# Performance work log

Measured on AMD Instinct MI355X. Metric: run time of the kernel, lower is better.

## Reference

```python
import jax, jax.numpy as jnp
import numpy as np

B, L, A, D = 16, 1024, 512, 1024


def setup_inputs() -> dict:
    key = jax.random.key(0)
    ks = jax.random.split(key, 12)
    s = 1.0 / np.sqrt(D)
    s2 = 1.0 / np.sqrt(2 * D)
    return {
        "text_features": jax.random.normal(ks[0], (B, L, D), jnp.float32),
        "audio_features": jax.random.normal(ks[1], (B, A, D), jnp.float32),
        "Wt1": jax.random.uniform(ks[2], (D, D), jnp.float32, -s, s),
        "bt1": jax.random.uniform(ks[3], (D,), jnp.float32, -s, s),
        "Wa1": jax.random.uniform(ks[4], (D, D), jnp.float32, -s, s),
        "w_att1": jax.random.uniform(ks[5], (2 * D,), jnp.float32, -s2, s2),
        "b_att1": jax.random.uniform(ks[6], (), jnp.float32, -s2, s2),
        "Wt2": jax.random.uniform(ks[7], (D, D), jnp.float32, -s, s),
        "Wa2": jax.random.uniform(ks[8], (D, D), jnp.float32, -s, s),
        "ba2": jax.random.uniform(ks[9], (D,), jnp.float32, -s, s),
        "w_att2": jax.random.uniform(ks[10], (2 * D,), jnp.float32, -s2, s2),
        "b_att2": jax.random.uniform(ks[11], (), jnp.float32, -s2, s2),
    }


def reference(text_features, audio_features, Wt1, bt1, Wa1, w_att1, b_att1,
              Wt2, Wa2, ba2, w_att2, b_att2):
    # Additive co-attention. tanh(cat([u_i, v_j])) = cat([tanh(u_i), tanh(v_j)]),
    # so the post-tanh linear score decomposes into an outer sum — exact same math
    # as the naive repeat/cat/tanh/linear, without the (B,L,A,2D) intermediate.
    d = Wt1.shape[0]
    # --- attention over audio regions ---
    u1 = jnp.tanh(jnp.einsum('bld,ed->ble', text_features, Wt1) + bt1)   # (B,L,D)
    v1 = jnp.tanh(jnp.einsum('bad,ed->bae', audio_features, Wa1))        # (B,A,D)
    scores1 = (u1 @ w_att1[:d])[:, :, None] + (v1 @ w_att1[d:])[:, None, :] + b_att1  # (B,L,A)
    audio_att = jax.nn.softmax(scores1, axis=-1)
    att_audio_features = jnp.einsum('bla,bad->bld', audio_att, audio_features)  # (B,L,D)
    # --- attention over text positions (self.args.max_seq_len == L) ---
    u2 = jnp.tanh(jnp.einsum('bld,ed->ble', att_audio_features, Wa2) + ba2)  # (B,L,D)
    v2 = jnp.tanh(jnp.einsum('bkd,ed->bke', text_features, Wt2))             # (B,L,D)
    scores2 = (u2 @ w_att2[:d])[:, :, None] + (v2 @ w_att2[d:])[:, None, :] + b_att2  # (B,L,L)
    textual_att = jax.nn.softmax(scores2, axis=-1)
    att_text_features = jnp.einsum('blk,bkd->bld', textual_att, text_features)
    return (att_text_features, att_audio_features)
```

## Files before the change

### kernel.cpp

```cpp
#include <hip/hip_runtime.h>

typedef unsigned short u16;
typedef float f32x4 __attribute__((ext_vector_type(4)));
typedef int   i32x4 __attribute__((ext_vector_type(4)));
typedef u16   u16x8 __attribute__((ext_vector_type(8)));

#define SWZ(i) ((i) ^ ((((i) >> 6) & 3) << 3))

__device__ __forceinline__ u16 f2bf(float f) {
  unsigned u = __float_as_uint(f);
  u += 0x7FFFu + ((u >> 16) & 1u);
  return (u16)(u >> 16);
}

__device__ __forceinline__ int cvt_pk_bf16(float lo, float hi) {
  int r;
  asm("v_cvt_pk_bf16_f32 %0, %1, %2" : "=v"(r) : "v"(lo), "v"(hi));
  return r;
}

__device__ __forceinline__ float tanh_fast(float x) {
  float e = __expf(2.0f * x);
  return 1.0f - 2.0f / (e + 1.0f);
}

__device__ __forceinline__ void mfma_bf16(f32x4& acc, i32x4 a, i32x4 b) {
  asm("v_mfma_f32_16x16x32_bf16 %0, %1, %2, %0" : "+v"(acc) : "v"(a), "v"(b));
}

__global__ __launch_bounds__(256) void wcast_kernel(
    const float* __restrict__ w2, const float* __restrict__ w1,
    u16* __restrict__ w2b, u16* __restrict__ w1b) {
  int i = blockIdx.x * 256 + threadIdx.x;
  const float* src; u16* dst; int j;
  if (i < 131072) { src = w2; dst = w2b; j = i; }
  else            { src = w1; dst = w1b; j = i - 131072; }
  const float4* s = (const float4*)src;
  float4 a = s[2 * j], b = s[2 * j + 1];
  u16x8 o;
  o[0] = f2bf(a.x); o[1] = f2bf(a.y); o[2] = f2bf(a.z); o[3] = f2bf(a.w);
  o[4] = f2bf(b.x); o[5] = f2bf(b.y); o[6] = f2bf(b.z); o[7] = f2bf(b.w);
  *(u16x8*)(dst + (size_t)8 * j) = o;
}

__global__ __launch_bounds__(256) void score_kernel(
    const float* __restrict__ audio, const u16* __restrict__ w1b,
    const float* __restrict__ wva, float* __restrict__ sva,
    const float* __restrict__ text, const u16* __restrict__ w2b,
    const float* __restrict__ wvt, float* __restrict__ svt) {
  __shared__ u16 At[128 * 32];
  __shared__ u16 Bt[128 * 32];

  int bx = blockIdx.x;
  const float* Xf; const u16* Wb_; const float* wv; float* svout; int mt, split, M;
  if (bx < 256) {
    Xf = audio; Wb_ = w1b; wv = wva; svout = sva; M = 8192;
    mt = (bx & 7) * 8 + (bx >> 5); split = (bx >> 3) & 3;
  } else {
    int x = bx - 256;
    Xf = text; Wb_ = w2b; wv = wvt; svout = svt; M = 16384;
    mt = (x & 7) * 16 + (x >> 5); split = (x >> 3) & 3;
  }

  const int t = threadIdx.x;
  const int wid = t >> 6, lane = t & 63;
  const int wm = wid >> 1, wn = wid & 1;
  const int lane15 = lane & 15, lg = lane >> 4;
  const size_t m_base = (size_t)mt * 128;

  float rs[4][4];
  #pragma unroll
  for (int mi = 0; mi < 4; ++mi)
    #pragma unroll
    for (int r = 0; r < 4; ++r) rs[mi][r] = 0.f;

  const int ar0 = t >> 2,        ac0 = (t & 3) * 8;
  const int ar1 = (256 + t) >> 2, ac1 = (t & 3) * 8;
  const int wiA0 = SWZ(ar0 * 32 + ac0), wiA1 = SWZ(ar1 * 32 + ac1);

  const float* Xb = Xf + m_base * 1024;

  for (int nt = 0; nt < 2; ++nt) {
    const int n0 = split * 256 + nt * 128;

    f32x4 acc[4][4];
    #pragma unroll
    for (int mi = 0; mi < 4; ++mi)
      #pragma unroll
      for (int ni = 0; ni < 4; ++ni)
        acc[mi][ni] = (f32x4){0.f, 0.f, 0.f, 0.f};

    const u16* Wp = Wb_ + (size_t)n0 * 1024;

    float4 xa0 = *(const float4*)(Xb + (size_t)ar0 * 1024 + ac0);
    float4 xa0b = *(const float4*)(Xb + (size_t)ar0 * 1024 + ac0 + 4);
    float4 xa1 = *(const float4*)(Xb + (size_t)ar1 * 1024 + ac1);
    float4 xa1b = *(const float4*)(Xb + (size_t)ar1 * 1024 + ac1 + 4);
    i32x4 rb0 = *(const i32x4*)(Wp + (size_t)ar0 * 1024 + ac0);
    i32x4 rb1 = *(const i32x4*)(Wp + (size_t)ar1 * 1024 + ac1);

    for (int kt = 0; kt < 32; ++kt) {
      i32x4 wa0, wa1;
      wa0[0] = cvt_pk_bf16(xa0.x, xa0.y);  wa0[1] = cvt_pk_bf16(xa0.z, xa0.w);
      wa0[2] = cvt_pk_bf16(xa0b.x, xa0b.y); wa0[3] = cvt_pk_bf16(xa0b.z, xa0b.w);
      wa1[0] = cvt_pk_bf16(xa1.x, xa1.y);  wa1[1] = cvt_pk_bf16(xa1.z, xa1.w);
      wa1[2] = cvt_pk_bf16(xa1b.x, xa1b.y); wa1[3] = cvt_pk_bf16(xa1b.z, xa1b.w);
      __syncthreads();
      *(i32x4*)(At + wiA0) = wa0;
      *(i32x4*)(At + wiA1) = wa1;
      *(i32x4*)(Bt + wiA0) = rb0;
      *(i32x4*)(Bt + wiA1) = rb1;
      __syncthreads();
      if (kt < 31) {
        const int k1 = (kt + 1) * 32;
        xa0  = *(const float4*)(Xb + (size_t)ar0 * 1024 + k1 + ac0);
        xa0b = *(const float4*)(Xb + (size_t)ar0 * 1024 + k1 + ac0 + 4);
        xa1  = *(const float4*)(Xb + (size_t)ar1 * 1024 + k1 + ac1);
        xa1b = *(const float4*)(Xb + (size_t)ar1 * 1024 + k1 + ac1 + 4);
        rb0  = *(const i32x4*)(Wp + (size_t)ar0 * 1024 + k1 + ac0);
        rb1  = *(const i32x4*)(Wp + (size_t)ar1 * 1024 + k1 + ac1);
      }
      i32x4 af[4], bfr[4];
      #pragma unroll
      for (int mi = 0; mi < 4; ++mi) {
        int rr = wm * 64 + mi * 16 + lane15;
        af[mi] = *(const i32x4*)(At + SWZ(rr * 32 + lg * 8));
      }
      #pragma unroll
      for (int ni = 0; ni < 4; ++ni) {
        int rr = wn * 64 + ni * 16 + lane15;
        bfr[ni] = *(const i32x4*)(Bt + SWZ(rr * 32 + lg * 8));
      }
      #pragma unroll
      for (int mi = 0; mi < 4; ++mi)
        #pragma unroll
        for (int ni = 0; ni < 4; ++ni)
          mfma_bf16(acc[mi][ni], af[mi], bfr[ni]);
    }

    float wvn[4];
    #pragma unroll
    for (int ni = 0; ni < 4; ++ni) wvn[ni] = wv[n0 + wn * 64 + ni * 16 + lane15];
    #pragma unroll
    for (int mi = 0; mi < 4; ++mi)
      #pragma unroll
      for (int ni = 0; ni < 4; ++ni)
        #pragma unroll
        for (int r = 0; r < 4; ++r)
          rs[mi][r] += tanh_fast(acc[mi][ni][r]) * wvn[ni];
  }

  __syncthreads();
  float* sred = (float*)At;
  #pragma unroll
  for (int mi = 0; mi < 4; ++mi)
    #pragma unroll
    for (int r = 0; r < 4; ++r) {
      float v = rs[mi][r];
      v += __shfl_xor(v, 1);
      v += __shfl_xor(v, 2);
      v += __shfl_xor(v, 4);
      v += __shfl_xor(v, 8);
      if (lane15 == 0) sred[wn * 128 + wm * 64 + mi * 16 + lg * 4 + r] = v;
    }
  __syncthreads();
  if (t < 128) svout[(size_t)split * M + m_base + t] = sred[t] + sred[128 + t];
}

__global__ __launch_bounds__(256) void softq_bcast_kernel(
    const float* __restrict__ xA, const float* __restrict__ svA,
    const float* __restrict__ xT, const float* __restrict__ svT,
    float* __restrict__ out) {
  int bx = blockIdx.x;
  int stage = bx >> 8;
  int b = (bx >> 4) & 15, dch = bx & 15;
  int Acnt = stage ? 1024 : 512;
  int M = stage ? 16384 : 8192;
  const float* x = stage ? xT : xA;
  const float* svp = stage ? svT : svA;
  int rowbase = b * Acnt;

  __shared__ float p[1024];
  __shared__ float red[256];
  __shared__ float chunk[64];
  int t = threadIdx.x;

  float mloc = -1e30f;
  for (int a = t; a < Acnt; a += 256) {
    float v = svp[rowbase + a] + svp[M + rowbase + a] +
              svp[2 * M + rowbase + a] + svp[3 * M + rowbase + a];
    p[a] = v;
    mloc = fmaxf(mloc, v);
  }
  #pragma unroll
  for (int off = 32; off; off >>= 1) mloc = fmaxf(mloc, __shfl_xor(mloc, off));
  if ((t & 63) == 0) red[t >> 6] = mloc;
  __syncthreads();
  float mx = fmaxf(fmaxf(red[0], red[1]), fmaxf(red[2], red[3]));

  float sloc = 0.f;
  for (int a = t; a < Acnt; a += 256) {
    float e = __expf(p[a] - mx);
    p[a] = e;
    sloc += e;
  }
  #pragma unroll
  for (int off = 32; off; off >>= 1) sloc += __shfl_xor(sloc, off);
  __syncthreads();
  if ((t & 63) == 0) red[t >> 6] = sloc;
  __syncthreads();
  float inv = 1.0f / (red[0] + red[1] + red[2] + red[3]);

  int dl = t & 63, ag = t >> 6;
  const float* xb = x + (size_t)rowbase * 1024 + dch * 64 + dl;
  float acc = 0.f;
  #pragma unroll 8
  for (int a = ag; a < Acnt; a += 4) acc += p[a] * xb[(size_t)a * 1024];
  __syncthreads();
  red[t] = acc;
  __syncthreads();
  if (t < 64) {
    float tot = red[t] + red[t + 64] + red[t + 128] + red[t + 192];
    chunk[t] = tot * inv;
  }
  __syncthreads();

  size_t base4 = ((stage ? (size_t)0 : (size_t)16777216) +
                  (size_t)b * 1048576 + (size_t)dch * 64) >> 2;
  f32x4* o4 = (f32x4*)out;
  f32x4 v = ((f32x4*)chunk)[t & 15];
  int q = t & 15;
  #pragma unroll 4
  for (int l = t >> 4; l < 1024; l += 16)
    __builtin_nontemporal_store(v, &o4[base4 + (size_t)l * 256 + q]);
}

extern "C" void kernel_launch(void* const* d_in, const int* in_sizes, int n_in,
                              void* d_out, int out_size, void* d_ws, size_t ws_size,
                              hipStream_t stream) {
  const float* text  = (const float*)d_in[0];
  const float* audio = (const float*)d_in[1];
  const float* Wa1   = (const float*)d_in[4];
  const float* watt1 = (const float*)d_in[5];
  const float* Wt2   = (const float*)d_in[7];
  const float* watt2 = (const float*)d_in[10];

  char* ws = (char*)d_ws;
  u16*   w2b = (u16*)(ws);
  u16*   w1b = (u16*)(ws + 2097152);
  float* sv2 = (float*)(ws + 4194304);
  float* sv1 = (float*)(ws + 4456448);

  wcast_kernel<<<1024, 256, 0, stream>>>(Wt2, Wa1, w2b, w1b);

  score_kernel<<<768, 256, 0, stream>>>(audio, w1b, watt1 + 1024, sv1,
                                        text, w2b, watt2 + 1024, sv2);

  softq_bcast_kernel<<<512, 256, 0, stream>>>(audio, sv1, text, sv2, (float*)d_out);
}
```

Before: 352.9 us.

## Double-buffer score GEMM LDS tiles and split N across twice as many blocks

The score kernel now stages its A and B tiles in double-buffered shared memory, so each k-step needs one barrier instead of two and the next tile's conversion and store overlap the current MFMAs. Each block now covers a single 128-wide N tile instead of two, which doubles the grid to 1536 blocks and produces 8 partial score vectors per row instead of 4. The softmax kernel sums the 8 partials and the workspace offset for the audio scores moves to fit them. The change also asks for 4 blocks per CU through launch bounds and drops the old block-index swizzle. In exchange, shared memory per block doubles, the X tile is re-read by twice as many blocks, and the partial-sum traffic doubles.

```diff
diff --git a/kernel.cpp b/kernel.cpp
--- a/kernel.cpp
+++ b/kernel.cpp
@@ -43,114 +43,120 @@
   *(u16x8*)(dst + (size_t)8 * j) = o;
 }
 
-__global__ __launch_bounds__(256) void score_kernel(
+__global__ __launch_bounds__(256, 4) void score_kernel(
     const float* __restrict__ audio, const u16* __restrict__ w1b,
     const float* __restrict__ wva, float* __restrict__ sva,
     const float* __restrict__ text, const u16* __restrict__ w2b,
     const float* __restrict__ wvt, float* __restrict__ svt) {
-  __shared__ u16 At[128 * 32];
-  __shared__ u16 Bt[128 * 32];
+  __shared__ u16 At[2][4096];
+  __shared__ u16 Bt[2][4096];
 
   int bx = blockIdx.x;
   const float* Xf; const u16* Wb_; const float* wv; float* svout; int mt, split, M;
-  if (bx < 256) {
+  if (bx < 512) {
     Xf = audio; Wb_ = w1b; wv = wva; svout = sva; M = 8192;
-    mt = (bx & 7) * 8 + (bx >> 5); split = (bx >> 3) & 3;
+    split = bx >> 6; mt = bx & 63;
   } else {
-    int x = bx - 256;
+    int x = bx - 512;
     Xf = text; Wb_ = w2b; wv = wvt; svout = svt; M = 16384;
-    mt = (x & 7) * 16 + (x >> 5); split = (x >> 3) & 3;
-  }
+    split = x >> 7; mt = x & 127;
+  }
+  const int n0 = split * 128;
 
   const int t = threadIdx.x;
   const int wid = t >> 6, lane = t & 63;
   const int wm = wid >> 1, wn = wid & 1;
   const int lane15 = lane & 15, lg = lane >> 4;
-  const size_t m_base = (size_t)mt * 128;
-
-  float rs[4][4];
+
+  const int ar0 = t >> 2,         ac0 = (t & 3) * 8;
+  const int ar1 = (256 + t) >> 2, ac1 = (t & 3) * 8;
+  const int wi0 = SWZ(ar0 * 32 + ac0), wi1 = SWZ(ar1 * 32 + ac1);
+
+  const float* Xb = Xf + (size_t)mt * 128 * 1024;
+  const u16*   Wp = Wb_ + (size_t)n0 * 1024;
+
+  f32x4 acc[4][4];
   #pragma unroll
   for (int mi = 0; mi < 4; ++mi)
     #pragma unroll
-    for (int r = 0; r < 4; ++r) rs[mi][r] = 0.f;
-
-  const int ar0 = t >> 2,        ac0 = (t & 3) * 8;
-  const int ar1 = (256 + t) >> 2, ac1 = (t & 3) * 8;
-  const int wiA0 = SWZ(ar0 * 32 + ac0), wiA1 = SWZ(ar1 * 32 + ac1);
-
-  const float* Xb = Xf + m_base * 1024;
-
-  for (int nt = 0; nt < 2; ++nt) {
-    const int n0 = split * 256 + nt * 128;
-
-    f32x4 acc[4][4];
+    for (int ni = 0; ni < 4; ++ni)
+      acc[mi][ni] = (f32x4){0.f, 0.f, 0.f, 0.f};
+
+  float4 xa0  = *(const float4*)(Xb + (size_t)ar0 * 1024 + ac0);
+  float4 xa0b = *(const float4*)(Xb + (size_t)ar0 * 1024 + ac0 + 4);
+  float4 xa1  = *(const float4*)(Xb + (size_t)ar1 * 1024 + ac1);
+  float4 xa1b = *(const float4*)(Xb + (size_t)ar1 * 1024 + ac1 + 4);
+  i32x4 rb0 = *(const i32x4*)(Wp + (size_t)ar0 * 1024 + ac0);
+  i32x4 rb1 = *(const i32x4*)(Wp + (size_t)ar1 * 1024 + ac1);
+  {
+    i32x4 wa0, wa1;
+    wa0[0] = cvt_pk_bf16(xa0.x, xa0.y);   wa0[1] = cvt_pk_bf16(xa0.z, xa0.w);
+    wa0[2] = cvt_pk_bf16(xa0b.x, xa0b.y); wa0[3] = cvt_pk_bf16(xa0b.z, xa0b.w);
+    wa1[0] = cvt_pk_bf16(xa1.x, xa1.y);   wa1[1] = cvt_pk_bf16(xa1.z, xa1.w);
+    wa1[2] = cvt_pk_bf16(xa1b.x, xa1b.y); wa1[3] = cvt_pk_bf16(xa1b.z, xa1b.w);
+    *(i32x4*)(At[0] + wi0) = wa0;
+    *(i32x4*)(At[0] + wi1) = wa1;
+    *(i32x4*)(Bt[0] + wi0) = rb0;
+    *(i32x4*)(Bt[0] + wi1) = rb1;
+  }
+  __syncthreads();
+
+  for (int kt = 0; kt < 32; ++kt) {
+    const int cur = kt & 1;
+    if (kt < 31) {
+      const int k1 = (kt + 1) * 32;
+      xa0  = *(const float4*)(Xb + (size_t)ar0 * 1024 + k1 + ac0);
+      xa0b = *(const float4*)(Xb + (size_t)ar0 * 1024 + k1 + ac0 + 4);
+      xa1  = *(const float4*)(Xb + (size_t)ar1 * 1024 + k1 + ac1);
+      xa1b = *(const float4*)(Xb + (size_t)ar1 * 1024 + k1 + ac1 + 4);
+      rb0  = *(const i32x4*)(Wp + (size_t)ar0 * 1024 + k1 + ac0);
+      rb1  = *(const i32x4*)(Wp + (size_t)ar1 * 1024 + k1 + ac1);
+    }
+    i32x4 af[4], bfr[4];
+    #pragma unroll
+    for (int mi = 0; mi < 4; ++mi) {
+      int rr = wm * 64 + mi * 16 + lane15;
+      af[mi] = *(const i32x4*)(At[cur] + SWZ(rr * 32 + lg * 8));
+    }
+    #pragma unroll
+    for (int ni = 0; ni < 4; ++ni) {
+      int rr = wn * 64 + ni * 16 + lane15;
+      bfr[ni] = *(const i32x4*)(Bt[cur] + SWZ(rr * 32 + lg * 8));
+    }
     #pragma unroll
     for (int mi = 0; mi < 4; ++mi)
       #pragma unroll
       for (int ni = 0; ni < 4; ++ni)
-        acc[mi][ni] = (f32x4){0.f, 0.f, 0.f, 0.f};
-
-    const u16* Wp = Wb_ + (size_t)n0 * 1024;
-
-    float4 xa0 = *(const float4*)(Xb + (size_t)ar0 * 1024 + ac0);
-    float4 xa0b = *(const float4*)(Xb + (size_t)ar0 * 1024 + ac0 + 4);
-    float4 xa1 = *(const float4*)(Xb + (size_t)ar1 * 1024 + ac1);
-    float4 xa1b = *(const float4*)(Xb + (size_t)ar1 * 1024 + ac1 + 4);
-    i32x4 rb0 = *(const i32x4*)(Wp + (size_t)ar0 * 1024 + ac0);
-    i32x4 rb1 = *(const i32x4*)(Wp + (size_t)ar1 * 1024 + ac1);
-
-    for (int kt = 0; kt < 32; ++kt) {
+        mfma_bf16(acc[mi][ni], af[mi], bfr[ni]);
+    if (kt < 31) {
       i32x4 wa0, wa1;
-      wa0[0] = cvt_pk_bf16(xa0.x, xa0.y);  wa0[1] = cvt_pk_bf16(xa0.z, xa0.w);
+      wa0[0] = cvt_pk_bf16(xa0.x, xa0.y);   wa0[1] = cvt_pk_bf16(xa0.z, xa0.w);
       wa0[2] = cvt_pk_bf16(xa0b.x, xa0b.y); wa0[3] = cvt_pk_bf16(xa0b.z, xa0b.w);
-      wa1[0] = cvt_pk_bf16(xa1.x, xa1.y);  wa1[1] = cvt_pk_bf16(xa1.z, xa1.w);
+      wa1[0] = cvt_pk_bf16(xa1.x, xa1.y);   wa1[1] = cvt_pk_bf16(xa1.z, xa1.w);
       wa1[2] = cvt_pk_bf16(xa1b.x, xa1b.y); wa1[3] = cvt_pk_bf16(xa1b.z, xa1b.w);
-      __syncthreads();
-      *(i32x4*)(At + wiA0) = wa0;
-      *(i32x4*)(At + wiA1) = wa1;
-      *(i32x4*)(Bt + wiA0) = rb0;
-      *(i32x4*)(Bt + wiA1) = rb1;
-      __syncthreads();
-      if (kt < 31) {
-        const int k1 = (kt + 1) * 32;
-        xa0  = *(const float4*)(Xb + (size_t)ar0 * 1024 + k1 + ac0);
-        xa0b = *(const float4*)(Xb + (size_t)ar0 * 1024 + k1 + ac0 + 4);
-        xa1  = *(const float4*)(Xb + (size_t)ar1 * 1024 + k1 + ac1);
-        xa1b = *(const float4*)(Xb + (size_t)ar1 * 1024 + k1 + ac1 + 4);
-        rb0  = *(const i32x4*)(Wp + (size_t)ar0 * 1024 + k1 + ac0);
-        rb1  = *(const i32x4*)(Wp + (size_t)ar1 * 1024 + k1 + ac1);
-      }
-      i32x4 af[4], bfr[4];
-      #pragma unroll
-      for (int mi = 0; mi < 4; ++mi) {
-        int rr = wm * 64 + mi * 16 + lane15;
-        af[mi] = *(const i32x4*)(At + SWZ(rr * 32 + lg * 8));
-      }
-      #pragma unroll
-      for (int ni = 0; ni < 4; ++ni) {
-        int rr = wn * 64 + ni * 16 + lane15;
-        bfr[ni] = *(const i32x4*)(Bt + SWZ(rr * 32 + lg * 8));
-      }
-      #pragma unroll
-      for (int mi = 0; mi < 4; ++mi)
-        #pragma unroll
-        for (int ni = 0; ni < 4; ++ni)
-          mfma_bf16(acc[mi][ni], af[mi], bfr[ni]);
-    }
-
-    float wvn[4];
-    #pragma unroll
-    for (int ni = 0; ni < 4; ++ni) wvn[ni] = wv[n0 + wn * 64 + ni * 16 + lane15];
-    #pragma unroll
-    for (int mi = 0; mi < 4; ++mi)
+      *(i32x4*)(At[cur ^ 1] + wi0) = wa0;
+      *(i32x4*)(At[cur ^ 1] + wi1) = wa1;
+      *(i32x4*)(Bt[cur ^ 1] + wi0) = rb0;
+      *(i32x4*)(Bt[cur ^ 1] + wi1) = rb1;
+    }
+    __syncthreads();
+  }
+
+  float wvn[4];
+  #pragma unroll
+  for (int ni = 0; ni < 4; ++ni) wvn[ni] = wv[n0 + wn * 64 + ni * 16 + lane15];
+  float rs[4][4];
+  #pragma unroll
+  for (int mi = 0; mi < 4; ++mi)
+    #pragma unroll
+    for (int r = 0; r < 4; ++r) {
+      float v = 0.f;
       #pragma unroll
       for (int ni = 0; ni < 4; ++ni)
-        #pragma unroll
-        for (int r = 0; r < 4; ++r)
-          rs[mi][r] += tanh_fast(acc[mi][ni][r]) * wvn[ni];
-  }
-
-  __syncthreads();
+        v += tanh_fast(acc[mi][ni][r]) * wvn[ni];
+      rs[mi][r] = v;
+    }
+
   float* sred = (float*)At;
   #pragma unroll
   for (int mi = 0; mi < 4; ++mi)
@@ -164,7 +170,7 @@
       if (lane15 == 0) sred[wn * 128 + wm * 64 + mi * 16 + lg * 4 + r] = v;
     }
   __syncthreads();
-  if (t < 128) svout[(size_t)split * M + m_base + t] = sred[t] + sred[128 + t];
+  if (t < 128) svout[(size_t)split * M + (size_t)mt * 128 + t] = sred[t] + sred[128 + t];
 }
 
 __global__ __launch_bounds__(256) void softq_bcast_kernel(
@@ -187,8 +193,9 @@
 
   float mloc = -1e30f;
   for (int a = t; a < Acnt; a += 256) {
-    float v = svp[rowbase + a] + svp[M + rowbase + a] +
-              svp[2 * M + rowbase + a] + svp[3 * M + rowbase + a];
+    float v = 0.f;
+    #pragma unroll
+    for (int s = 0; s < 8; ++s) v += svp[s * M + rowbase + a];
     p[a] = v;
     mloc = fmaxf(mloc, v);
   }
@@ -249,12 +256,12 @@
   u16*   w2b = (u16*)(ws);
   u16*   w1b = (u16*)(ws + 2097152);
   float* sv2 = (float*)(ws + 4194304);
-  float* sv1 = (float*)(ws + 4456448);
+  float* sv1 = (float*)(ws + 4718592);
 
   wcast_kernel<<<1024, 256, 0, stream>>>(Wt2, Wa1, w2b, w1b);
 
-  score_kernel<<<768, 256, 0, stream>>>(audio, w1b, watt1 + 1024, sv1,
-                                        text, w2b, watt2 + 1024, sv2);
+  score_kernel<<<1536, 256, 0, stream>>>(audio, w1b, watt1 + 1024, sv1,
+                                         text, w2b, watt2 + 1024, sv2);
 
   softq_bcast_kernel<<<512, 256, 0, stream>>>(audio, sv1, text, sv2, (float*)d_out);
 }
```

After: 364.9 us. 3.4% more time.
